# Kernel tuning notes

Measured on AMD Instinct MI355X. Metric: run time of the kernel, lower is better.

## Reference

```python
import jax, jax.numpy as jnp
import numpy as np

B, N, C, H = 16, 1024, 512, 8
HD = C // H
SCALE = HD ** -0.5
EPS = 1e-5
THRESH = 1.0


def _bn(y, gamma, beta):
    # y: [B, N, C]; BatchNorm1d over channel C -> reduce over (B, N) (training-mode batch stats)
    mean = y.mean(axis=(0, 1))
    var = y.var(axis=(0, 1))  # biased variance, as torch uses for normalization
    return gamma * (y - mean) * jax.lax.rsqrt(var + EPS) + beta


def _spike(u):
    # single-step LIF with zero initial membrane: spk = heaviside(beta*0 + u - threshold)
    return (u > THRESH).astype(u.dtype)


def setup_inputs() -> dict:
    key = jax.random.key(0)
    ks = jax.random.split(key, 11)
    s = C ** -0.5
    return {
        "x": jax.random.normal(ks[0], (B, N, C), dtype=jnp.float32),
        "Wq": jax.random.normal(ks[1], (C, C), dtype=jnp.float32) * s,
        "Wk": jax.random.normal(ks[2], (C, C), dtype=jnp.float32) * s,
        "Wv": jax.random.normal(ks[3], (C, C), dtype=jnp.float32) * s,
        "Wo": jax.random.normal(ks[4], (C, C), dtype=jnp.float32) * s,
        "q_gamma": jnp.ones((C,), jnp.float32),
        "q_beta": jnp.zeros((C,), jnp.float32),
        "k_gamma": jnp.ones((C,), jnp.float32),
        "k_beta": jnp.zeros((C,), jnp.float32),
        "v_gamma": jnp.ones((C,), jnp.float32),
        "v_beta": jnp.zeros((C,), jnp.float32),
    }


def reference(x, Wq, Wk, Wv, Wo, q_gamma, q_beta, k_gamma, k_beta, v_gamma, v_beta):
    def branch(W, g, b):
        return _spike(_bn(x @ W.T, g, b))  # [B, N, C], binary spikes

    q = branch(Wq, q_gamma, q_beta).reshape(B, N, H, HD).transpose(0, 2, 1, 3)
    k = branch(Wk, k_gamma, k_beta).reshape(B, N, H, HD).transpose(0, 2, 1, 3)
    v = branch(Wv, v_gamma, v_beta).reshape(B, N, H, HD).transpose(0, 2, 1, 3)

    # softmax-free attention: (q k^T) v * scale
    attn = jnp.einsum("bhnd,bhmd->bhnm", q, k) * SCALE  # [B, H, N, N]
    out = jnp.einsum("bhnm,bhmd->bhnd", attn, v)        # [B, H, N, HD]
    out = out.transpose(0, 2, 1, 3).reshape(B, N, C)
    return out @ Wo.T
```

## Files before the change

### kernel.cpp

```cpp
#include <hip/hip_runtime.h>
#include <hip/hip_bf16.h>
#include <cstdint>
#include <cstddef>

#define M_ROWS 16384
#define CDIM   512
#define HEADS  8
#define HD     64
#define NSEQ   1024
#define BATCH  16
#define NPART  256

typedef _Float16 h8 __attribute__((ext_vector_type(8)));
typedef float f4 __attribute__((ext_vector_type(4)));

__device__ __forceinline__ void split8(float4 u, float4 v, h8& hi, h8& lo) {
  float t[8] = {u.x, u.y, u.z, u.w, v.x, v.y, v.z, v.w};
  #pragma unroll
  for (int e = 0; e < 8; ++e) {
    _Float16 h = (_Float16)t[e];
    hi[e] = h;
    lo[e] = (_Float16)((t[e] - (float)h) * 2048.0f);
  }
}

__global__ __launch_bounds__(256, 2) void gemm16(
    const float* __restrict__ A,
    const float* __restrict__ W0, const float* __restrict__ W1, const float* __restrict__ W2,
    float* __restrict__ C0, float* __restrict__ C1, float* __restrict__ C2,
    int K, int ldc)
{
  const float* W = (blockIdx.z == 0) ? W0 : (blockIdx.z == 1) ? W1 : W2;
  float* Cm      = (blockIdx.z == 0) ? C0 : (blockIdx.z == 1) ? C1 : C2;

  __shared__ _Float16 sAh[128][40], sAl[128][40], sBh[128][40], sBl[128][40];

  const int tid = threadIdx.x;
  const int bm = blockIdx.y * 128;
  const int bn = blockIdx.x * 128;
  const int srow = tid >> 1;
  const int skq  = (tid & 1) * 16;

  const int ln = tid & 63;
  const int wr = ((tid >> 6) >> 1) * 64;
  const int wc = ((tid >> 6) & 1) * 64;
  const int fr = ln & 15;
  const int fk = (ln >> 4) * 8;

  f4 acc1[4][4], acc2[4][4];
  #pragma unroll
  for (int i = 0; i < 4; ++i)
    #pragma unroll
    for (int j = 0; j < 4; ++j) { acc1[i][j] = 0.f; acc2[i][j] = 0.f; }

  const float* ga = A + (size_t)(bm + srow) * K + skq;
  const float* gb = W + (size_t)(bn + srow) * K + skq;

  float4 a0 = *(const float4*)(ga + 0),  a1 = *(const float4*)(ga + 4);
  float4 a2 = *(const float4*)(ga + 8),  a3 = *(const float4*)(ga + 12);
  float4 b0 = *(const float4*)(gb + 0),  b1 = *(const float4*)(gb + 4);
  float4 b2 = *(const float4*)(gb + 8),  b3 = *(const float4*)(gb + 12);

  for (int k0 = 0; k0 < K; k0 += 32) {
    h8 hA0, lA0, hA1, lA1, hB0, lB0, hB1, lB1;
    split8(a0, a1, hA0, lA0); split8(a2, a3, hA1, lA1);
    split8(b0, b1, hB0, lB0); split8(b2, b3, hB1, lB1);
    __syncthreads();
    *(h8*)&sAh[srow][skq] = hA0; *(h8*)&sAh[srow][skq + 8] = hA1;
    *(h8*)&sAl[srow][skq] = lA0; *(h8*)&sAl[srow][skq + 8] = lA1;
    *(h8*)&sBh[srow][skq] = hB0; *(h8*)&sBh[srow][skq + 8] = hB1;
    *(h8*)&sBl[srow][skq] = lB0; *(h8*)&sBl[srow][skq + 8] = lB1;
    __syncthreads();

    if (k0 + 32 < K) {
      const float* pa = ga + k0 + 32;
      a0 = *(const float4*)(pa + 0);  a1 = *(const float4*)(pa + 4);
      a2 = *(const float4*)(pa + 8);  a3 = *(const float4*)(pa + 12);
      const float* pb = gb + k0 + 32;
      b0 = *(const float4*)(pb + 0);  b1 = *(const float4*)(pb + 4);
      b2 = *(const float4*)(pb + 8);  b3 = *(const float4*)(pb + 12);
    }

    h8 bhf[4], blf[4];
    #pragma unroll
    for (int j = 0; j < 4; ++j) {
      bhf[j] = *(const h8*)&sBh[wc + j * 16 + fr][fk];
      blf[j] = *(const h8*)&sBl[wc + j * 16 + fr][fk];
    }
    #pragma unroll
    for (int i = 0; i < 4; ++i) {
      h8 ah = *(const h8*)&sAh[wr + i * 16 + fr][fk];
      h8 al = *(const h8*)&sAl[wr + i * 16 + fr][fk];
      #pragma unroll
      for (int j = 0; j < 4; ++j) {
        acc1[i][j] = __builtin_amdgcn_mfma_f32_16x16x32_f16(ah, bhf[j], acc1[i][j], 0, 0, 0);
        acc2[i][j] = __builtin_amdgcn_mfma_f32_16x16x32_f16(ah, blf[j], acc2[i][j], 0, 0, 0);
        acc2[i][j] = __builtin_amdgcn_mfma_f32_16x16x32_f16(al, bhf[j], acc2[i][j], 0, 0, 0);
      }
    }
  }

  const int orow = (ln >> 4) * 4;
  #pragma unroll
  for (int i = 0; i < 4; ++i)
    #pragma unroll
    for (int j = 0; j < 4; ++j) {
      float* cp = Cm + (size_t)(bm + wr + i * 16 + orow) * ldc + (bn + wc + j * 16 + fr);
      #pragma unroll
      for (int r = 0; r < 4; ++r)
        cp[(size_t)r * ldc] = acc1[i][j][r] + acc2[i][j][r] * 4.8828125e-4f;
    }
}

__global__ __launch_bounds__(256) void stats_partial(const float* __restrict__ y,
                                                     float* __restrict__ partial)
{
  const int branch = blockIdx.y;
  const int chunk = blockIdx.x;
  const int t = threadIdx.x;
  const int sub = t >> 7;
  const int c4 = t & 127;
  const float* yb = y + (size_t)branch * M_ROWS * CDIM
                      + (size_t)(chunk * 128 + sub * 64) * CDIM + c4 * 4;

  float s[4] = {0.f, 0.f, 0.f, 0.f}, q[4] = {0.f, 0.f, 0.f, 0.f};
  for (int r = 0; r < 64; ++r) {
    float4 v = *(const float4*)(yb + (size_t)r * CDIM);
    s[0] += v.x; q[0] += v.x * v.x;
    s[1] += v.y; q[1] += v.y * v.y;
    s[2] += v.z; q[2] += v.z * v.z;
    s[3] += v.w; q[3] += v.w * v.w;
  }
  const int pr = chunk * 2 + sub;
  float2* pb = (float2*)partial + ((size_t)branch * NPART + pr) * CDIM + c4 * 4;
  #pragma unroll
  for (int j = 0; j < 4; ++j) pb[j] = make_float2(s[j], q[j]);
}

__global__ void finalize_stats(const float* __restrict__ partial, float* __restrict__ ab,
                               const float* __restrict__ g0, const float* __restrict__ b0,
                               const float* __restrict__ g1, const float* __restrict__ b1,
                               const float* __restrict__ g2, const float* __restrict__ b2)
{
  const int branch = blockIdx.x;
  const int c = threadIdx.x;
  const float* g  = branch == 0 ? g0 : branch == 1 ? g1 : g2;
  const float* be = branch == 0 ? b0 : branch == 1 ? b1 : b2;

  float sum = 0.f, sq = 0.f;
  const float2* pb = (const float2*)partial + (size_t)branch * NPART * CDIM + c;
  for (int pr = 0; pr < NPART; ++pr) {
    float2 v = pb[(size_t)pr * CDIM];
    sum += v.x; sq += v.y;
  }
  const float invn = 1.f / (float)M_ROWS;
  float mean = sum * invn;
  float var  = sq * invn - mean * mean;
  float rsig = rsqrtf(var + 1e-5f);
  ((float2*)ab)[branch * CDIM + c] = make_float2(g[c] * rsig, be[c] - g[c] * mean * rsig);
}

__global__ __launch_bounds__(256) void fixup_kernel(
    float* __restrict__ y, const float* __restrict__ ab,
    const float* __restrict__ x,
    const float* __restrict__ Wq, const float* __restrict__ Wk,
    const float* __restrict__ Wv)
{
  const size_t total = (size_t)3 * M_ROWS * CDIM;
  const size_t stride = (size_t)gridDim.x * blockDim.x * 4;
  for (size_t i4 = ((size_t)blockIdx.x * blockDim.x + threadIdx.x) * 4;
       i4 < total; i4 += stride) {
    float4 v = *(const float4*)(y + i4);
    float vv[4] = {v.x, v.y, v.z, v.w};
    const int c0 = (int)(i4 & (CDIM - 1));
    const int branch = (int)(i4 / ((size_t)M_ROWS * CDIM));
    const float2* abb = (const float2*)ab + branch * CDIM;
    #pragma unroll
    for (int u = 0; u < 4; ++u) {
      float2 ab2 = abb[c0 + u];
      float t = vv[u] * ab2.x + ab2.y;
      if (fabsf(t - 1.0f) < 1e-4f) {
        size_t rem = (i4 + u) - (size_t)branch * M_ROWS * CDIM;
        int m = (int)(rem >> 9);
        int c = (int)(rem & (CDIM - 1));
        const float* Wp = branch == 0 ? Wq : branch == 1 ? Wk : Wv;
        const float* xr = x + (size_t)m * CDIM;
        const float* wrow = Wp + (size_t)c * CDIM;
        float acc = 0.f;
        for (int k = 0; k < CDIM; ++k) acc = fmaf(xr[k], wrow[k], acc);
        y[i4 + u] = acc;
      }
    }
  }
}

__global__ __launch_bounds__(256) void kv_kernel(const float* __restrict__ kraw,
                                                 const float* __restrict__ vraw,
                                                 const float* __restrict__ ab,
                                                 float* __restrict__ KV)
{
  const int b = blockIdx.z, h = blockIdx.y, mc = blockIdx.x;
  __shared__ float ks[64][64];
  __shared__ float vs[64][64];
  __shared__ float ka_s[64], kb_s[64], va_s[64], vb_s[64];
  const int t = threadIdx.x;

  if (t < 64) {
    float2 kab = ((const float2*)ab)[1 * CDIM + h * HD + t];
    ka_s[t] = kab.x; kb_s[t] = kab.y;
  } else if (t < 128) {
    int j = t - 64;
    float2 vab = ((const float2*)ab)[2 * CDIM + h * HD + j];
    va_s[j] = vab.x; vb_s[j] = vab.y;
  }
  __syncthreads();

  const size_t base = ((size_t)(b * NSEQ + mc * 64)) * CDIM + h * HD;
  #pragma unroll
  for (int i = 0; i < 4; ++i) {
    int f = t + i * 256;
    int row = f >> 4, c4 = f & 15;
    float4 kv4 = *(const float4*)(kraw + base + (size_t)row * CDIM + c4 * 4);
    float4 vv4 = *(const float4*)(vraw + base + (size_t)row * CDIM + c4 * 4);
    int c = c4 * 4;
    kv4.x = (kv4.x * ka_s[c+0] + kb_s[c+0] > 1.0f) ? 1.f : 0.f;
    kv4.y = (kv4.y * ka_s[c+1] + kb_s[c+1] > 1.0f) ? 1.f : 0.f;
    kv4.z = (kv4.z * ka_s[c+2] + kb_s[c+2] > 1.0f) ? 1.f : 0.f;
    kv4.w = (kv4.w * ka_s[c+3] + kb_s[c+3] > 1.0f) ? 1.f : 0.f;
    vv4.x = (vv4.x * va_s[c+0] + vb_s[c+0] > 1.0f) ? 1.f : 0.f;
    vv4.y = (vv4.y * va_s[c+1] + vb_s[c+1] > 1.0f) ? 1.f : 0.f;
    vv4.z = (vv4.z * va_s[c+2] + vb_s[c+2] > 1.0f) ? 1.f : 0.f;
    vv4.w = (vv4.w * va_s[c+3] + vb_s[c+3] > 1.0f) ? 1.f : 0.f;
    *(float4*)&ks[row][c4 * 4] = kv4;
    *(float4*)&vs[row][c4 * 4] = vv4;
  }
  __syncthreads();

  const int d = t & 63;
  const int dp0 = (t >> 6) * 16;
  float acc[16];
  #pragma unroll
  for (int j = 0; j < 16; ++j) acc[j] = 0.f;

  for (int m = 0; m < 64; ++m) {
    float vv = vs[m][d];
    #pragma unroll
    for (int q4 = 0; q4 < 4; ++q4) {
      float4 kf = *(const float4*)&ks[m][dp0 + q4 * 4];
      acc[q4 * 4 + 0] = fmaf(kf.x, vv, acc[q4 * 4 + 0]);
      acc[q4 * 4 + 1] = fmaf(kf.y, vv, acc[q4 * 4 + 1]);
      acc[q4 * 4 + 2] = fmaf(kf.z, vv, acc[q4 * 4 + 2]);
      acc[q4 * 4 + 3] = fmaf(kf.w, vv, acc[q4 * 4 + 3]);
    }
  }
  float* kvb = KV + ((size_t)(b * HEADS + h)) * HD * HD;
  #pragma unroll
  for (int j = 0; j < 16; ++j)
    atomicAdd(&kvb[(dp0 + j) * HD + d], acc[j]);
}

__global__ __launch_bounds__(256) void qkv_kernel(const float* __restrict__ qraw,
                                                  const float* __restrict__ ab,
                                                  const float* __restrict__ KV,
                                                  float* __restrict__ out1)
{
  const int b = blockIdx.z, h = blockIdx.y, rc = blockIdx.x;
  __shared__ float kvs[64][64];
  __shared__ float qs[128][64];
  __shared__ float qa_s[64], qb_s[64];
  const int t = threadIdx.x;

  if (t < 64) {
    float2 qab = ((const float2*)ab)[0 * CDIM + h * HD + t];
    qa_s[t] = qab.x; qb_s[t] = qab.y;
  }
  __syncthreads();

  const float* kvb = KV + ((size_t)(b * HEADS + h)) * HD * HD;
  #pragma unroll
  for (int i = 0; i < 4; ++i) {
    int f = t + i * 256;
    int row = f >> 4, c4 = f & 15;
    *(float4*)&kvs[row][c4 * 4] = *(const float4*)(kvb + row * 64 + c4 * 4);
  }
  const size_t qbase = ((size_t)(b * NSEQ + rc * 128)) * CDIM + h * HD;
  #pragma unroll
  for (int i = 0; i < 8; ++i) {
    int f = t + i * 256;
    int row = f >> 4, c4 = f & 15;
    float4 v = *(const float4*)(qraw + qbase + (size_t)row * CDIM + c4 * 4);
    int c = c4 * 4;
    v.x = (v.x * qa_s[c+0] + qb_s[c+0] > 1.0f) ? 1.f : 0.f;
    v.y = (v.y * qa_s[c+1] + qb_s[c+1] > 1.0f) ? 1.f : 0.f;
    v.z = (v.z * qa_s[c+2] + qb_s[c+2] > 1.0f) ? 1.f : 0.f;
    v.w = (v.w * qa_s[c+3] + qb_s[c+3] > 1.0f) ? 1.f : 0.f;
    *(float4*)&qs[row][c4 * 4] = v;
  }
  __syncthreads();

  const int d = t & 63;
  const int rg = t >> 6;
  for (int r = rg * 32; r < rg * 32 + 32; ++r) {
    float acc = 0.f;
    #pragma unroll
    for (int dq = 0; dq < 16; ++dq) {
      float4 qf = *(const float4*)&qs[r][dq * 4];
      acc = fmaf(qf.x, kvs[dq * 4 + 0][d], acc);
      acc = fmaf(qf.y, kvs[dq * 4 + 1][d], acc);
      acc = fmaf(qf.z, kvs[dq * 4 + 2][d], acc);
      acc = fmaf(qf.w, kvs[dq * 4 + 3][d], acc);
    }
    out1[((size_t)(b * NSEQ + rc * 128 + r)) * CDIM + h * HD + d] = acc * 0.125f;
  }
}

extern "C" void kernel_launch(void* const* d_in, const int* in_sizes, int n_in,
                              void* d_out, int out_size, void* d_ws, size_t ws_size,
                              hipStream_t stream)
{
  const float* x  = (const float*)d_in[0];
  const float* Wq = (const float*)d_in[1];
  const float* Wk = (const float*)d_in[2];
  const float* Wv = (const float*)d_in[3];
  const float* Wo = (const float*)d_in[4];
  const float* qg = (const float*)d_in[5];
  const float* qb = (const float*)d_in[6];
  const float* kg = (const float*)d_in[7];
  const float* kb = (const float*)d_in[8];
  const float* vg = (const float*)d_in[9];
  const float* vb = (const float*)d_in[10];
  float* out = (float*)d_out;

  char* ws = (char*)d_ws;
  const size_t ybytes  = (size_t)M_ROWS * CDIM * sizeof(float);
  const size_t pbytes  = (size_t)3 * NPART * CDIM * 2 * sizeof(float);
  const size_t abbytes = (size_t)3 * CDIM * 2 * sizeof(float);
  const size_t kvbytes = (size_t)BATCH * HEADS * HD * HD * sizeof(float);
  const size_t need = 3 * ybytes + pbytes + abbytes + kvbytes;

  if (ws_size < need) return;

  float* yq      = (float*)(ws);
  float* yk      = (float*)(ws + ybytes);
  float* yv      = (float*)(ws + 2 * ybytes);
  float* partial = (float*)(ws + 3 * ybytes);
  float* ab      = (float*)(ws + 3 * ybytes + pbytes);
  float* KV      = (float*)(ws + 3 * ybytes + pbytes + abbytes);
  float* out1    = yk;

  hipMemsetAsync(KV, 0, kvbytes, stream);

  gemm16<<<dim3(CDIM / 128, M_ROWS / 128, 3), 256, 0, stream>>>(
      x, Wq, Wk, Wv, yq, yk, yv, CDIM, CDIM);

  stats_partial<<<dim3(NPART / 2, 3), 256, 0, stream>>>(yq, partial);
  finalize_stats<<<3, CDIM, 0, stream>>>(partial, ab, qg, qb, kg, kb, vg, vb);

  fixup_kernel<<<2048, 256, 0, stream>>>(yq, ab, x, Wq, Wk, Wv);

  kv_kernel<<<dim3(NSEQ / 64, HEADS, BATCH), 256, 0, stream>>>(yk, yv, ab, KV);

  qkv_kernel<<<dim3(NSEQ / 128, HEADS, BATCH), 256, 0, stream>>>(yq, ab, KV, out1);

  gemm16<<<dim3(CDIM / 128, M_ROWS / 128, 1), 256, 0, stream>>>(
      out1, Wo, Wo, Wo, out, out, out, CDIM, CDIM);
}
```

Before: 378.9 us.

## Fuse near-threshold fixup into attention kernels and XOR-swizzle GEMM LDS

Removes the standalone fixup pass that re-read all three projection outputs (about 100MB) and folds the exact-dot-product recompute for near-threshold values into the spike conversion inside kv_kernel and qkv_kernel. It also drops the padded shared-memory rows in the split-fp16 GEMM in favour of an XOR swizzle on the column index, to avoid bank conflicts with less LDS. Trade-offs: the rare slow path now runs inside the attention kernels and can cause wave divergence, and the swizzle adds index arithmetic.

```diff
diff --git a/kernel.cpp b/kernel.cpp
--- a/kernel.cpp
+++ b/kernel.cpp
@@ -24,6 +24,18 @@
   }
 }
 
+__device__ __forceinline__ float spike_or_exact(float raw, float a, float b,
+                                                const float* __restrict__ xr,
+                                                const float* __restrict__ wrow) {
+  float t = raw * a + b;
+  if (__builtin_expect(fabsf(t - 1.0f) < 1e-4f, 0)) {
+    float acc = 0.f;
+    for (int k = 0; k < CDIM; ++k) acc = fmaf(xr[k], wrow[k], acc);
+    t = acc * a + b;
+  }
+  return t > 1.0f ? 1.f : 0.f;
+}
+
 __global__ __launch_bounds__(256, 2) void gemm16(
     const float* __restrict__ A,
     const float* __restrict__ W0, const float* __restrict__ W1, const float* __restrict__ W2,
@@ -33,13 +45,14 @@
   const float* W = (blockIdx.z == 0) ? W0 : (blockIdx.z == 1) ? W1 : W2;
   float* Cm      = (blockIdx.z == 0) ? C0 : (blockIdx.z == 1) ? C1 : C2;
 
-  __shared__ _Float16 sAh[128][40], sAl[128][40], sBh[128][40], sBl[128][40];
+  __shared__ _Float16 sAh[128][32], sAl[128][32], sBh[128][32], sBl[128][32];
 
   const int tid = threadIdx.x;
   const int bm = blockIdx.y * 128;
   const int bn = blockIdx.x * 128;
   const int srow = tid >> 1;
-  const int skq  = (tid & 1) * 16;
+  const int scol = (tid & 1) * 16;
+  const int sc1  = scol ^ (((srow >> 1) & 3) << 3);
 
   const int ln = tid & 63;
   const int wr = ((tid >> 6) >> 1) * 64;
@@ -53,8 +66,8 @@
     #pragma unroll
     for (int j = 0; j < 4; ++j) { acc1[i][j] = 0.f; acc2[i][j] = 0.f; }
 
-  const float* ga = A + (size_t)(bm + srow) * K + skq;
-  const float* gb = W + (size_t)(bn + srow) * K + skq;
+  const float* ga = A + (size_t)(bm + srow) * K + scol;
+  const float* gb = W + (size_t)(bn + srow) * K + scol;
 
   float4 a0 = *(const float4*)(ga + 0),  a1 = *(const float4*)(ga + 4);
   float4 a2 = *(const float4*)(ga + 8),  a3 = *(const float4*)(ga + 12);
@@ -66,10 +79,10 @@
     split8(a0, a1, hA0, lA0); split8(a2, a3, hA1, lA1);
     split8(b0, b1, hB0, lB0); split8(b2, b3, hB1, lB1);
     __syncthreads();
-    *(h8*)&sAh[srow][skq] = hA0; *(h8*)&sAh[srow][skq + 8] = hA1;
-    *(h8*)&sAl[srow][skq] = lA0; *(h8*)&sAl[srow][skq + 8] = lA1;
-    *(h8*)&sBh[srow][skq] = hB0; *(h8*)&sBh[srow][skq + 8] = hB1;
-    *(h8*)&sBl[srow][skq] = lB0; *(h8*)&sBl[srow][skq + 8] = lB1;
+    *(h8*)&sAh[srow][sc1] = hA0; *(h8*)&sAh[srow][sc1 ^ 8] = hA1;
+    *(h8*)&sAl[srow][sc1] = lA0; *(h8*)&sAl[srow][sc1 ^ 8] = lA1;
+    *(h8*)&sBh[srow][sc1] = hB0; *(h8*)&sBh[srow][sc1 ^ 8] = hB1;
+    *(h8*)&sBl[srow][sc1] = lB0; *(h8*)&sBl[srow][sc1 ^ 8] = lB1;
     __syncthreads();
 
     if (k0 + 32 < K) {
@@ -84,13 +97,17 @@
     h8 bhf[4], blf[4];
     #pragma unroll
     for (int j = 0; j < 4; ++j) {
-      bhf[j] = *(const h8*)&sBh[wc + j * 16 + fr][fk];
-      blf[j] = *(const h8*)&sBl[wc + j * 16 + fr][fk];
+      const int rowB = wc + j * 16 + fr;
+      const int cB = fk ^ (((rowB >> 1) & 3) << 3);
+      bhf[j] = *(const h8*)&sBh[rowB][cB];
+      blf[j] = *(const h8*)&sBl[rowB][cB];
     }
     #pragma unroll
     for (int i = 0; i < 4; ++i) {
-      h8 ah = *(const h8*)&sAh[wr + i * 16 + fr][fk];
-      h8 al = *(const h8*)&sAl[wr + i * 16 + fr][fk];
+      const int rowA = wr + i * 16 + fr;
+      const int cA = fk ^ (((rowA >> 1) & 3) << 3);
+      h8 ah = *(const h8*)&sAh[rowA][cA];
+      h8 al = *(const h8*)&sAl[rowA][cA];
       #pragma unroll
       for (int j = 0; j < 4; ++j) {
         acc1[i][j] = __builtin_amdgcn_mfma_f32_16x16x32_f16(ah, bhf[j], acc1[i][j], 0, 0, 0);
@@ -160,43 +177,12 @@
   ((float2*)ab)[branch * CDIM + c] = make_float2(g[c] * rsig, be[c] - g[c] * mean * rsig);
 }
 
-__global__ __launch_bounds__(256) void fixup_kernel(
-    float* __restrict__ y, const float* __restrict__ ab,
-    const float* __restrict__ x,
-    const float* __restrict__ Wq, const float* __restrict__ Wk,
-    const float* __restrict__ Wv)
-{
-  const size_t total = (size_t)3 * M_ROWS * CDIM;
-  const size_t stride = (size_t)gridDim.x * blockDim.x * 4;
-  for (size_t i4 = ((size_t)blockIdx.x * blockDim.x + threadIdx.x) * 4;
-       i4 < total; i4 += stride) {
-    float4 v = *(const float4*)(y + i4);
-    float vv[4] = {v.x, v.y, v.z, v.w};
-    const int c0 = (int)(i4 & (CDIM - 1));
-    const int branch = (int)(i4 / ((size_t)M_ROWS * CDIM));
-    const float2* abb = (const float2*)ab + branch * CDIM;
-    #pragma unroll
-    for (int u = 0; u < 4; ++u) {
-      float2 ab2 = abb[c0 + u];
-      float t = vv[u] * ab2.x + ab2.y;
-      if (fabsf(t - 1.0f) < 1e-4f) {
-        size_t rem = (i4 + u) - (size_t)branch * M_ROWS * CDIM;
-        int m = (int)(rem >> 9);
-        int c = (int)(rem & (CDIM - 1));
-        const float* Wp = branch == 0 ? Wq : branch == 1 ? Wk : Wv;
-        const float* xr = x + (size_t)m * CDIM;
-        const float* wrow = Wp + (size_t)c * CDIM;
-        float acc = 0.f;
-        for (int k = 0; k < CDIM; ++k) acc = fmaf(xr[k], wrow[k], acc);
-        y[i4 + u] = acc;
-      }
-    }
-  }
-}
-
 __global__ __launch_bounds__(256) void kv_kernel(const float* __restrict__ kraw,
                                                  const float* __restrict__ vraw,
                                                  const float* __restrict__ ab,
+                                                 const float* __restrict__ x,
+                                                 const float* __restrict__ Wk,
+                                                 const float* __restrict__ Wv,
                                                  float* __restrict__ KV)
 {
   const int b = blockIdx.z, h = blockIdx.y, mc = blockIdx.x;
@@ -223,14 +209,17 @@
     float4 kv4 = *(const float4*)(kraw + base + (size_t)row * CDIM + c4 * 4);
     float4 vv4 = *(const float4*)(vraw + base + (size_t)row * CDIM + c4 * 4);
     int c = c4 * 4;
-    kv4.x = (kv4.x * ka_s[c+0] + kb_s[c+0] > 1.0f) ? 1.f : 0.f;
-    kv4.y = (kv4.y * ka_s[c+1] + kb_s[c+1] > 1.0f) ? 1.f : 0.f;
-    kv4.z = (kv4.z * ka_s[c+2] + kb_s[c+2] > 1.0f) ? 1.f : 0.f;
-    kv4.w = (kv4.w * ka_s[c+3] + kb_s[c+3] > 1.0f) ? 1.f : 0.f;
-    vv4.x = (vv4.x * va_s[c+0] + vb_s[c+0] > 1.0f) ? 1.f : 0.f;
-    vv4.y = (vv4.y * va_s[c+1] + vb_s[c+1] > 1.0f) ? 1.f : 0.f;
-    vv4.z = (vv4.z * va_s[c+2] + vb_s[c+2] > 1.0f) ? 1.f : 0.f;
-    vv4.w = (vv4.w * va_s[c+3] + vb_s[c+3] > 1.0f) ? 1.f : 0.f;
+    const float* xr = x + (size_t)(b * NSEQ + mc * 64 + row) * CDIM;
+    const float* wk0 = Wk + (size_t)(h * HD + c) * CDIM;
+    const float* wv0 = Wv + (size_t)(h * HD + c) * CDIM;
+    kv4.x = spike_or_exact(kv4.x, ka_s[c+0], kb_s[c+0], xr, wk0);
+    kv4.y = spike_or_exact(kv4.y, ka_s[c+1], kb_s[c+1], xr, wk0 + CDIM);
+    kv4.z = spike_or_exact(kv4.z, ka_s[c+2], kb_s[c+2], xr, wk0 + 2 * CDIM);
+    kv4.w = spike_or_exact(kv4.w, ka_s[c+3], kb_s[c+3], xr, wk0 + 3 * CDIM);
+    vv4.x = spike_or_exact(vv4.x, va_s[c+0], vb_s[c+0], xr, wv0);
+    vv4.y = spike_or_exact(vv4.y, va_s[c+1], vb_s[c+1], xr, wv0 + CDIM);
+    vv4.z = spike_or_exact(vv4.z, va_s[c+2], vb_s[c+2], xr, wv0 + 2 * CDIM);
+    vv4.w = spike_or_exact(vv4.w, va_s[c+3], vb_s[c+3], xr, wv0 + 3 * CDIM);
     *(float4*)&ks[row][c4 * 4] = kv4;
     *(float4*)&vs[row][c4 * 4] = vv4;
   }
@@ -262,6 +251,8 @@
 __global__ __launch_bounds__(256) void qkv_kernel(const float* __restrict__ qraw,
                                                   const float* __restrict__ ab,
                                                   const float* __restrict__ KV,
+                                                  const float* __restrict__ x,
+                                                  const float* __restrict__ Wq,
                                                   float* __restrict__ out1)
 {
   const int b = blockIdx.z, h = blockIdx.y, rc = blockIdx.x;
@@ -290,10 +281,12 @@
     int row = f >> 4, c4 = f & 15;
     float4 v = *(const float4*)(qraw + qbase + (size_t)row * CDIM + c4 * 4);
     int c = c4 * 4;
-    v.x = (v.x * qa_s[c+0] + qb_s[c+0] > 1.0f) ? 1.f : 0.f;
-    v.y = (v.y * qa_s[c+1] + qb_s[c+1] > 1.0f) ? 1.f : 0.f;
-    v.z = (v.z * qa_s[c+2] + qb_s[c+2] > 1.0f) ? 1.f : 0.f;
-    v.w = (v.w * qa_s[c+3] + qb_s[c+3] > 1.0f) ? 1.f : 0.f;
+    const float* xr = x + (size_t)(b * NSEQ + rc * 128 + row) * CDIM;
+    const float* wq0 = Wq + (size_t)(h * HD + c) * CDIM;
+    v.x = spike_or_exact(v.x, qa_s[c+0], qb_s[c+0], xr, wq0);
+    v.y = spike_or_exact(v.y, qa_s[c+1], qb_s[c+1], xr, wq0 + CDIM);
+    v.z = spike_or_exact(v.z, qa_s[c+2], qb_s[c+2], xr, wq0 + 2 * CDIM);
+    v.w = spike_or_exact(v.w, qa_s[c+3], qb_s[c+3], xr, wq0 + 3 * CDIM);
     *(float4*)&qs[row][c4 * 4] = v;
   }
   __syncthreads();
@@ -356,11 +349,11 @@
   stats_partial<<<dim3(NPART / 2, 3), 256, 0, stream>>>(yq, partial);
   finalize_stats<<<3, CDIM, 0, stream>>>(partial, ab, qg, qb, kg, kb, vg, vb);
 
-  fixup_kernel<<<2048, 256, 0, stream>>>(yq, ab, x, Wq, Wk, Wv);
-
-  kv_kernel<<<dim3(NSEQ / 64, HEADS, BATCH), 256, 0, stream>>>(yk, yv, ab, KV);
-
-  qkv_kernel<<<dim3(NSEQ / 128, HEADS, BATCH), 256, 0, stream>>>(yq, ab, KV, out1);
+  kv_kernel<<<dim3(NSEQ / 64, HEADS, BATCH), 256, 0, stream>>>(
+      yk, yv, ab, x, Wk, Wv, KV);
+
+  qkv_kernel<<<dim3(NSEQ / 128, HEADS, BATCH), 256, 0, stream>>>(
+      yq, ab, KV, x, Wq, out1);
 
   gemm16<<<dim3(CDIM / 128, M_ROWS / 128, 1), 256, 0, stream>>>(
       out1, Wo, Wo, Wo, out, out, out, CDIM, CDIM);
```

New measurement: 373.8 us. No clear change (-1.3%).
